# Optimization experiments

Measured on AMD Instinct MI355X. Metric: run time of the kernel, lower is better.

## Reference

```python
import jax, jax.numpy as jnp
import numpy as np

N_NODES = 50000
N_EDGES = 800000
D_IN = 256
D_OUT = 256
N_REL = 8


def setup_inputs() -> dict:
    key = jax.random.key(0)
    k_x, k_ei, k_et, k_w = jax.random.split(key, 4)
    x = jax.random.normal(k_x, (N_NODES, D_IN), dtype=jnp.float32)
    edge_index = jax.random.randint(k_ei, (2, N_EDGES), 0, N_NODES, dtype=jnp.int32)
    edge_type = jax.random.randint(k_et, (N_EDGES,), 0, N_REL, dtype=jnp.int32)
    # xavier_uniform-style init for per-relation weights [R, I, O]
    limit = float(np.sqrt(6.0 / (D_IN + D_OUT)))
    weight = jax.random.uniform(k_w, (N_REL, D_IN, D_OUT), dtype=jnp.float32,
                                minval=-limit, maxval=limit)
    bias = jnp.zeros((D_OUT,), dtype=jnp.float32)
    return {"x": x, "edge_index": edge_index, "edge_type": edge_type,
            "weight": weight, "bias": bias}


def reference(x, edge_index, edge_type, weight, bias):
    # RGCN (block / per-relation weights):
    #   out[row] += x[col] @ weight[edge_type]
    # Vectorized: transform every node under every relation once (dense GEMM),
    # then gather the right (relation, col) slice per edge and scatter-add to row.
    num_nodes = x.shape[0]
    row, col = edge_index[0], edge_index[1]
    xt = jnp.einsum('ni,rio->rno', x, weight)          # [R, N, O]
    messages = xt[edge_type, col]                       # [E, O]
    out = jax.ops.segment_sum(messages, row, num_segments=num_nodes)  # [N, O]
    return jax.nn.relu(out + bias)
```

## Files before the change

kernel.cpp:

```cpp
#include <hip/hip_runtime.h>
#include <hip/hip_bf16.h>
#include <stdint.h>

typedef __attribute__((ext_vector_type(8))) short short8;
typedef __attribute__((ext_vector_type(4))) float f32x4;

#define D 256
#define NTY 4

static __device__ __forceinline__ float b2f(unsigned short u) {
  union { unsigned u; float f; } c; c.u = ((unsigned)u) << 16; return c.f;
}
static __device__ __forceinline__ unsigned short f2b(float f) {
  union { float f; unsigned u; } c; c.f = f;
  unsigned r = (c.u + 0x7FFFu + ((c.u >> 16) & 1u)) >> 16;
  return (unsigned short)r;
}

static __device__ __forceinline__ void gload16(const void* g, void* l) {
  __builtin_amdgcn_global_load_lds(
      (const __attribute__((address_space(1))) unsigned int*)g,
      (__attribute__((address_space(3))) unsigned int*)l, 16, 0, 0);
}

__global__ void k_cvt_xw(const float* __restrict__ x, unsigned short* __restrict__ xb,
                         long n_elems, long pad_elems, int xblocks,
                         const float* __restrict__ w, unsigned short* __restrict__ wt) {
  if (blockIdx.x < (unsigned)xblocks) {
    long i4 = (long)blockIdx.x * 256 + threadIdx.x;
    if (i4 * 4 >= pad_elems) return;
    ushort4 o;
    if (i4 * 4 < n_elems) {
      float4 v = ((const float4*)x)[i4];
      o.x = f2b(v.x); o.y = f2b(v.y); o.z = f2b(v.z); o.w = f2b(v.w);
    } else {
      o.x = 0; o.y = 0; o.z = 0; o.w = 0;
    }
    ((ushort4*)xb)[i4] = o;
  } else {
    int t = (blockIdx.x - xblocks) * 256 + threadIdx.x;
    int i = t & 255;
    int orow = t >> 8;
    int r = orow >> 8, o = orow & 255;
    wt[t] = f2b(w[((size_t)(r * 256 + i)) * 256 + o]);
  }
}

__global__ __launch_bounds__(256) void k_gemm(const unsigned short* __restrict__ A,
                                              const unsigned short* __restrict__ B,
                                              unsigned short* __restrict__ C,
                                              int ldc) {
  __shared__ __align__(16) char lA[64 * 512];
  __shared__ __align__(16) char lB[128 * 128];
  const int t = threadIdx.x;
  const int lane = t & 63;
  const int wave = t >> 6;
  const int l15 = lane & 15, lhi = lane >> 4;
  const size_t tm = (size_t)blockIdx.x * 64;
  const int y0 = blockIdx.y * NTY;

#pragma unroll
  for (int it = 0; it < 8; ++it) {
    int s = it * 256 + t;
    int row = s >> 5, c = s & 31;
    gload16(A + (tm + row) * 256 + ((c ^ (row & 7)) * 8),
            lA + (it * 256 + wave * 64) * 16);
  }

  for (int y = y0; y < y0 + NTY; ++y) {
    const int tn = y * 128;
    f32x4 acc[4][2];
#pragma unroll
    for (int a = 0; a < 4; ++a)
#pragma unroll
      for (int b = 0; b < 2; ++b)
#pragma unroll
        for (int e = 0; e < 4; ++e) acc[a][b][e] = 0.f;

    for (int kt = 0; kt < 256; kt += 64) {
      __syncthreads();
#pragma unroll
      for (int it = 0; it < 4; ++it) {
        int s = it * 256 + t;
        int row = s >> 3, c = s & 7;
        gload16(B + (tn + row) * 256 + kt + ((c ^ (row & 7)) * 8),
                lB + (it * 256 + wave * 64) * 16);
      }
      __syncthreads();

      short8 af[4][2], bfv[2][2];
      const int ktc = kt >> 3;
#pragma unroll
      for (int mi = 0; mi < 4; ++mi) {
#pragma unroll
        for (int kk = 0; kk < 2; ++kk) {
          int R = mi * 16 + l15;
          int c = ktc + kk * 4 + lhi;
          af[mi][kk] = *(const short8*)(lA + R * 512 + ((c ^ (R & 7)) * 16));
        }
      }
#pragma unroll
      for (int ni = 0; ni < 2; ++ni) {
#pragma unroll
        for (int kk = 0; kk < 2; ++kk) {
          int R2 = wave * 32 + ni * 16 + l15;
          int c2 = kk * 4 + lhi;
          bfv[ni][kk] = *(const short8*)(lB + R2 * 128 + ((c2 ^ (R2 & 7)) * 16));
        }
      }
#pragma unroll
      for (int mi = 0; mi < 4; ++mi) {
#pragma unroll
        for (int ni = 0; ni < 2; ++ni) {
          acc[mi][ni] = __builtin_amdgcn_mfma_f32_16x16x32_bf16(af[mi][0], bfv[ni][0], acc[mi][ni], 0, 0, 0);
          acc[mi][ni] = __builtin_amdgcn_mfma_f32_16x16x32_bf16(af[mi][1], bfv[ni][1], acc[mi][ni], 0, 0, 0);
        }
      }
    }
#pragma unroll
    for (int mi = 0; mi < 4; ++mi) {
#pragma unroll
      for (int j = 0; j < 4; ++j) {
        size_t row = tm + mi * 16 + lhi * 4 + j;
        unsigned pk = (unsigned)f2b(acc[mi][0][j]) | ((unsigned)f2b(acc[mi][1][j]) << 16);
        *(unsigned*)(C + row * (size_t)ldc + tn + wave * 32 + l15 * 2) = pk;
      }
    }
  }
}

__global__ void k_deg(const int* __restrict__ ei, int* deg, int E) {
  int e = blockIdx.x * 256 + threadIdx.x;
  if (e < E) atomicAdd(&deg[ei[e]], 1);
}
__global__ void k_scan1(const int* __restrict__ deg, int* bsum, int n) {
  __shared__ int sm[256];
  int t = threadIdx.x, idx = blockIdx.x * 256 + t;
  sm[t] = idx < n ? deg[idx] : 0;
  __syncthreads();
  for (int off = 128; off; off >>= 1) {
    if (t < off) sm[t] += sm[t + off];
    __syncthreads();
  }
  if (t == 0) bsum[blockIdx.x] = sm[0];
}
__global__ void k_scan23(const int* __restrict__ deg, const int* __restrict__ bsum,
                         int* rowptr, int* cursor, int nsc, int n) {
  __shared__ int sb[256];
  __shared__ int sm[256];
  int t = threadIdx.x, idx = blockIdx.x * 256 + t;
  int bv = t < nsc ? bsum[t] : 0;
  sb[t] = bv;
  __syncthreads();
  for (int off = 1; off < 256; off <<= 1) {
    int x = t >= off ? sb[t - off] : 0;
    __syncthreads();
    sb[t] += x;
    __syncthreads();
  }
  int v = idx < n ? deg[idx] : 0;
  sm[t] = v;
  __syncthreads();
  for (int off = 1; off < 256; off <<= 1) {
    int x = t >= off ? sm[t - off] : 0;
    __syncthreads();
    sm[t] += x;
    __syncthreads();
  }
  int boff = sb[blockIdx.x] - bsum[blockIdx.x];
  if (idx < n) {
    int e = boff + sm[t] - v;
    rowptr[idx] = e;
    cursor[idx] = e;
  }
  if (blockIdx.x == 0 && t == 0) rowptr[n] = sb[nsc - 1];
}
__global__ void k_bin(const int* __restrict__ ei, const int* __restrict__ et,
                      int* cursor, unsigned* ect, int E) {
  int e = blockIdx.x * 256 + threadIdx.x;
  if (e >= E) return;
  int r = ei[e], c = ei[E + e], ty = et[e];
  int pos = atomicAdd(&cursor[r], 1);
  ect[pos] = (unsigned)c | ((unsigned)ty << 20);
}

__global__ __launch_bounds__(256) void k_gather(const unsigned* __restrict__ ect,
                                                const int* __restrict__ rowptr,
                                                const unsigned short* __restrict__ xt,
                                                const float* __restrict__ bias,
                                                float* __restrict__ out, int n, int ldxt) {
  __shared__ float sm[4][256];
  const int lane = threadIdx.x & 63;
  const int wid = threadIdx.x >> 6;
  const int h = lane >> 5;
  const int sl = lane & 31;
  const int row = blockIdx.x * 4 + wid;
  if (row >= n) return;
  const int s = rowptr[row], e = rowptr[row + 1];
  const int cnt = e - s;
  float a[8] = {0.f, 0.f, 0.f, 0.f, 0.f, 0.f, 0.f, 0.f};
  unsigned myct = (s + lane < e) ? ect[s + lane] : 0u;
  int c1 = cnt > 64 ? 64 : cnt;
  for (int i = 0; i < c1; i += 2) {
    int j = i + h;
    unsigned ct = __shfl(myct, j);
    if (j < c1) {
      size_t base = (size_t)(ct & 0xFFFFFu) * ldxt + ((ct >> 20) << 8) + (sl << 3);
      short8 v = *(const short8*)(xt + base);
#pragma unroll
      for (int k = 0; k < 8; ++k) a[k] += b2f((unsigned short)v[k]);
    }
  }
  for (int i = s + 64; i < e; i += 2) {
    int j = i + h;
    if (j < e) {
      unsigned ct = ect[j];
      size_t base = (size_t)(ct & 0xFFFFFu) * ldxt + ((ct >> 20) << 8) + (sl << 3);
      short8 v = *(const short8*)(xt + base);
#pragma unroll
      for (int k = 0; k < 8; ++k) a[k] += b2f((unsigned short)v[k]);
    }
  }
#pragma unroll
  for (int k = 0; k < 8; ++k) a[k] += __shfl_xor(a[k], 32);
  if (h == 0) {
#pragma unroll
    for (int k = 0; k < 8; ++k) {
      int p8 = sl * 8 + k;
      int o = (p8 & 224) | ((p8 & 1) << 4) | ((p8 & 31) >> 1);
      sm[wid][o] = a[k];
    }
  }
  float4 v = *(const float4*)&sm[wid][lane * 4];
  float4 bb = ((const float4*)bias)[lane];
  float4 o;
  o.x = fmaxf(v.x + bb.x, 0.f);
  o.y = fmaxf(v.y + bb.y, 0.f);
  o.z = fmaxf(v.z + bb.z, 0.f);
  o.w = fmaxf(v.w + bb.w, 0.f);
  ((float4*)out)[(size_t)row * 64 + lane] = o;
}

extern "C" void kernel_launch(void* const* d_in, const int* in_sizes, int n_in,
                              void* d_out, int out_size, void* d_ws, size_t ws_size,
                              hipStream_t stream) {
  const float* x = (const float*)d_in[0];
  const int* ei = (const int*)d_in[1];
  const int* et = (const int*)d_in[2];
  const float* w = (const float*)d_in[3];
  const float* bias = (const float*)d_in[4];
  float* out = (float*)d_out;

  const int Nn = in_sizes[0] / D;
  const int E = in_sizes[2];
  const int R = in_sizes[3] / (D * D);
  const int Mpad = ((Nn + 63) / 64) * 64;
  const int NC = R * D;

  char* p = (char*)d_ws;
  auto alloc = [&](size_t bytes) -> char* {
    char* q = p;
    p += (bytes + 255) & ~(size_t)255;
    return q;
  };
  unsigned short* xt = (unsigned short*)alloc((size_t)Mpad * NC * 2);
  unsigned short* xb = (unsigned short*)alloc((size_t)Mpad * D * 2);
  unsigned short* wt = (unsigned short*)alloc((size_t)NC * D * 2);
  int* rowptr = (int*)alloc((size_t)(Nn + 1) * 4);
  int* cursor = (int*)alloc((size_t)Nn * 4);
  int* deg = (int*)alloc((size_t)Nn * 4);
  int* bsum = (int*)alloc(1024);
  unsigned* ect = (unsigned*)alloc((size_t)E * 4);

  const int nsc = (Nn + 255) / 256;
  const int xblocks = Mpad / 4;

  hipMemsetAsync(deg, 0, (size_t)Nn * 4, stream);
  hipLaunchKernelGGL(k_deg, dim3((E + 255) / 256), dim3(256), 0, stream, ei, deg, E);
  hipLaunchKernelGGL(k_scan1, dim3(nsc), dim3(256), 0, stream, deg, bsum, Nn);
  hipLaunchKernelGGL(k_scan23, dim3(nsc), dim3(256), 0, stream, deg, bsum,
                     rowptr, cursor, nsc, Nn);
  hipLaunchKernelGGL(k_bin, dim3((E + 255) / 256), dim3(256), 0, stream, ei, et, cursor, ect, E);

  hipLaunchKernelGGL(k_cvt_xw, dim3(xblocks + (NC * D) / 256), dim3(256), 0, stream,
                     x, xb, (long)Nn * D, (long)Mpad * D, xblocks, w, wt);
  hipLaunchKernelGGL(k_gemm, dim3(Mpad / 64, NC / (128 * NTY)), dim3(256), 0, stream,
                     xb, wt, xt, NC);

  hipLaunchKernelGGL(k_gather, dim3((Nn + 3) / 4), dim3(256), 0, stream, ect, rowptr,
                     xt, bias, out, Nn, NC);
}
```

Before: 356.2 us.

## Aggregate per relation before transform and fuse gather with per-relation GEMM

Reorders the computation from transform-then-gather to gather-then-transform. Edges are binned by (destination, relation) in a CSR built over N*R keys. A fused kernel sums bf16 input rows per relation for 32 destination nodes, stages them in LDS, and multiplies by that relation's weight with MFMA, accumulating across all 8 relations. This removes the large [N, R*256] bf16 intermediate write and its random re-read. The costs are an 8x larger degree/scan array, a serial per-thread edge loop inside the GEMM kernel, an extra bf16 rounding of the partial sums, and reloading the full weight matrix for every 32-row block.

```diff
diff --git a/kernel.cpp b/kernel.cpp
--- a/kernel.cpp
+++ b/kernel.cpp
@@ -6,15 +6,13 @@
 typedef __attribute__((ext_vector_type(4))) float f32x4;
 
 #define D 256
-#define NTY 4
 
 static __device__ __forceinline__ float b2f(unsigned short u) {
   union { unsigned u; float f; } c; c.u = ((unsigned)u) << 16; return c.f;
 }
-static __device__ __forceinline__ unsigned short f2b(float f) {
+static __device__ __forceinline__ unsigned f2b(float f) {
   union { float f; unsigned u; } c; c.f = f;
-  unsigned r = (c.u + 0x7FFFu + ((c.u >> 16) & 1u)) >> 16;
-  return (unsigned short)r;
+  return (c.u + 0x7FFFu + ((c.u >> 16) & 1u)) >> 16;
 }
 
 static __device__ __forceinline__ void gload16(const void* g, void* l) {
@@ -42,203 +40,191 @@
     int i = t & 255;
     int orow = t >> 8;
     int r = orow >> 8, o = orow & 255;
-    wt[t] = f2b(w[((size_t)(r * 256 + i)) * 256 + o]);
-  }
-}
-
-__global__ __launch_bounds__(256) void k_gemm(const unsigned short* __restrict__ A,
-                                              const unsigned short* __restrict__ B,
-                                              unsigned short* __restrict__ C,
-                                              int ldc) {
-  __shared__ __align__(16) char lA[64 * 512];
-  __shared__ __align__(16) char lB[128 * 128];
+    wt[t] = (unsigned short)f2b(w[((size_t)(r * 256 + i)) * 256 + o]);
+  }
+}
+
+__global__ void k_deg2(const int* __restrict__ ei, const int* __restrict__ et,
+                       int* deg, int E) {
+  int e = blockIdx.x * 256 + threadIdx.x;
+  if (e < E) atomicAdd(&deg[ei[e] * 8 + et[e]], 1);
+}
+__global__ void k_scan1(const int* __restrict__ deg, int* bsum, int n) {
+  __shared__ int sm[256];
+  int t = threadIdx.x, idx = blockIdx.x * 256 + t;
+  sm[t] = idx < n ? deg[idx] : 0;
+  __syncthreads();
+  for (int off = 128; off; off >>= 1) {
+    if (t < off) sm[t] += sm[t + off];
+    __syncthreads();
+  }
+  if (t == 0) bsum[blockIdx.x] = sm[0];
+}
+__global__ void k_scan2b(const int* __restrict__ bsum, int* __restrict__ boff,
+                         int* __restrict__ rp_end, int nsc) {
+  __shared__ int sm[256];
+  int t = threadIdx.x;
+  int loc[8];
+  int s = 0;
+#pragma unroll
+  for (int j = 0; j < 8; ++j) {
+    int idx = t * 8 + j;
+    loc[j] = s;
+    s += (idx < nsc) ? bsum[idx] : 0;
+  }
+  sm[t] = s;
+  __syncthreads();
+  for (int off = 1; off < 256; off <<= 1) {
+    int x = t >= off ? sm[t - off] : 0;
+    __syncthreads();
+    sm[t] += x;
+    __syncthreads();
+  }
+  int base = sm[t] - s;
+#pragma unroll
+  for (int j = 0; j < 8; ++j) {
+    int idx = t * 8 + j;
+    if (idx < nsc) boff[idx] = base + loc[j];
+  }
+  if (t == 255) *rp_end = sm[255];
+}
+__global__ void k_scan3(const int* __restrict__ deg, const int* __restrict__ boff,
+                        int* rowptr, int* cursor, int n) {
+  __shared__ int sm[256];
+  int t = threadIdx.x, idx = blockIdx.x * 256 + t;
+  int v = idx < n ? deg[idx] : 0;
+  sm[t] = v;
+  __syncthreads();
+  for (int off = 1; off < 256; off <<= 1) {
+    int x = t >= off ? sm[t - off] : 0;
+    __syncthreads();
+    sm[t] += x;
+    __syncthreads();
+  }
+  if (idx < n) {
+    int e = boff[blockIdx.x] + sm[t] - v;
+    rowptr[idx] = e;
+    cursor[idx] = e;
+  }
+}
+__global__ void k_bin2(const int* __restrict__ ei, const int* __restrict__ et,
+                       int* cursor, int* ecol, int E) {
+  int e = blockIdx.x * 256 + threadIdx.x;
+  if (e >= E) return;
+  int key = ei[e] * 8 + et[e];
+  int pos = atomicAdd(&cursor[key], 1);
+  ecol[pos] = ei[E + e];
+}
+
+__global__ __launch_bounds__(256) void k_fused(const unsigned short* __restrict__ xb,
+                                               const unsigned short* __restrict__ Wt,
+                                               const int* __restrict__ rp2,
+                                               const int* __restrict__ ecol,
+                                               const float* __restrict__ bias,
+                                               float* __restrict__ out, int Nn) {
+  __shared__ __align__(16) char lds[32 * 512 + 256 * 128];
+  char* lH = lds;
+  char* lB = lds + 32 * 512;
   const int t = threadIdx.x;
   const int lane = t & 63;
   const int wave = t >> 6;
   const int l15 = lane & 15, lhi = lane >> 4;
-  const size_t tm = (size_t)blockIdx.x * 64;
-  const int y0 = blockIdx.y * NTY;
-
-#pragma unroll
-  for (int it = 0; it < 8; ++it) {
-    int s = it * 256 + t;
-    int row = s >> 5, c = s & 31;
-    gload16(A + (tm + row) * 256 + ((c ^ (row & 7)) * 8),
-            lA + (it * 256 + wave * 64) * 16);
-  }
-
-  for (int y = y0; y < y0 + NTY; ++y) {
-    const int tn = y * 128;
-    f32x4 acc[4][2];
-#pragma unroll
-    for (int a = 0; a < 4; ++a)
-#pragma unroll
-      for (int b = 0; b < 2; ++b)
-#pragma unroll
-        for (int e = 0; e < 4; ++e) acc[a][b][e] = 0.f;
-
+  const int half = lane >> 5, sl = lane & 31;
+  const int tm = blockIdx.x * 32;
+
+  f32x4 acc[2][4];
+#pragma unroll
+  for (int a = 0; a < 2; ++a)
+#pragma unroll
+    for (int b = 0; b < 4; ++b)
+#pragma unroll
+      for (int e = 0; e < 4; ++e) acc[a][b][e] = 0.f;
+
+  for (int r = 0; r < 8; ++r) {
+    __syncthreads();
+#pragma unroll
+    for (int pr = 0; pr < 4; ++pr) {
+      int hr = wave * 8 + pr * 2 + half;
+      int row = tm + hr;
+      float a[8] = {0.f, 0.f, 0.f, 0.f, 0.f, 0.f, 0.f, 0.f};
+      if (row < Nn) {
+        int key = row * 8 + r;
+        int s = rp2[key], e = rp2[key + 1];
+        for (int i = s; i < e; ++i) {
+          int col = ecol[i];
+          short8 v = *(const short8*)(xb + (size_t)col * 256 + sl * 8);
+#pragma unroll
+          for (int k = 0; k < 8; ++k) a[k] += b2f((unsigned short)v[k]);
+        }
+      }
+      uint4 pk;
+      pk.x = f2b(a[0]) | (f2b(a[1]) << 16);
+      pk.y = f2b(a[2]) | (f2b(a[3]) << 16);
+      pk.z = f2b(a[4]) | (f2b(a[5]) << 16);
+      pk.w = f2b(a[6]) | (f2b(a[7]) << 16);
+      *(uint4*)(lH + hr * 512 + ((sl ^ (hr & 7)) * 16)) = pk;
+    }
     for (int kt = 0; kt < 256; kt += 64) {
       __syncthreads();
 #pragma unroll
-      for (int it = 0; it < 4; ++it) {
-        int s = it * 256 + t;
-        int row = s >> 3, c = s & 7;
-        gload16(B + (tn + row) * 256 + kt + ((c ^ (row & 7)) * 8),
+      for (int it = 0; it < 8; ++it) {
+        int s2 = it * 256 + t;
+        int nrow = s2 >> 3, c = s2 & 7;
+        gload16(Wt + ((size_t)(r * 256 + nrow)) * 256 + kt + ((c ^ (nrow & 7)) * 8),
                 lB + (it * 256 + wave * 64) * 16);
       }
       __syncthreads();
 
-      short8 af[4][2], bfv[2][2];
       const int ktc = kt >> 3;
-#pragma unroll
-      for (int mi = 0; mi < 4; ++mi) {
+      short8 af[2][2];
+#pragma unroll
+      for (int mi = 0; mi < 2; ++mi)
 #pragma unroll
         for (int kk = 0; kk < 2; ++kk) {
           int R = mi * 16 + l15;
           int c = ktc + kk * 4 + lhi;
-          af[mi][kk] = *(const short8*)(lA + R * 512 + ((c ^ (R & 7)) * 16));
+          af[mi][kk] = *(const short8*)(lH + R * 512 + ((c ^ (R & 7)) * 16));
+        }
+#pragma unroll
+      for (int ni = 0; ni < 4; ++ni) {
+        int R2 = wave * 64 + ni * 16 + l15;
+        short8 b0 = *(const short8*)(lB + R2 * 128 + ((lhi ^ (R2 & 7)) * 16));
+        short8 b1 = *(const short8*)(lB + R2 * 128 + (((4 + lhi) ^ (R2 & 7)) * 16));
+#pragma unroll
+        for (int mi = 0; mi < 2; ++mi) {
+          acc[mi][ni] = __builtin_amdgcn_mfma_f32_16x16x32_bf16(af[mi][0], b0, acc[mi][ni], 0, 0, 0);
+          acc[mi][ni] = __builtin_amdgcn_mfma_f32_16x16x32_bf16(af[mi][1], b1, acc[mi][ni], 0, 0, 0);
         }
       }
-#pragma unroll
-      for (int ni = 0; ni < 2; ++ni) {
-#pragma unroll
-        for (int kk = 0; kk < 2; ++kk) {
-          int R2 = wave * 32 + ni * 16 + l15;
-          int c2 = kk * 4 + lhi;
-          bfv[ni][kk] = *(const short8*)(lB + R2 * 128 + ((c2 ^ (R2 & 7)) * 16));
-        }
-      }
-#pragma unroll
-      for (int mi = 0; mi < 4; ++mi) {
-#pragma unroll
-        for (int ni = 0; ni < 2; ++ni) {
-          acc[mi][ni] = __builtin_amdgcn_mfma_f32_16x16x32_bf16(af[mi][0], bfv[ni][0], acc[mi][ni], 0, 0, 0);
-          acc[mi][ni] = __builtin_amdgcn_mfma_f32_16x16x32_bf16(af[mi][1], bfv[ni][1], acc[mi][ni], 0, 0, 0);
-        }
-      }
-    }
-#pragma unroll
-    for (int mi = 0; mi < 4; ++mi) {
-#pragma unroll
-      for (int j = 0; j < 4; ++j) {
-        size_t row = tm + mi * 16 + lhi * 4 + j;
-        unsigned pk = (unsigned)f2b(acc[mi][0][j]) | ((unsigned)f2b(acc[mi][1][j]) << 16);
-        *(unsigned*)(C + row * (size_t)ldc + tn + wave * 32 + l15 * 2) = pk;
-      }
-    }
-  }
-}
-
-__global__ void k_deg(const int* __restrict__ ei, int* deg, int E) {
-  int e = blockIdx.x * 256 + threadIdx.x;
-  if (e < E) atomicAdd(&deg[ei[e]], 1);
-}
-__global__ void k_scan1(const int* __restrict__ deg, int* bsum, int n) {
-  __shared__ int sm[256];
-  int t = threadIdx.x, idx = blockIdx.x * 256 + t;
-  sm[t] = idx < n ? deg[idx] : 0;
-  __syncthreads();
-  for (int off = 128; off; off >>= 1) {
-    if (t < off) sm[t] += sm[t + off];
-    __syncthreads();
-  }
-  if (t == 0) bsum[blockIdx.x] = sm[0];
-}
-__global__ void k_scan23(const int* __restrict__ deg, const int* __restrict__ bsum,
-                         int* rowptr, int* cursor, int nsc, int n) {
-  __shared__ int sb[256];
-  __shared__ int sm[256];
-  int t = threadIdx.x, idx = blockIdx.x * 256 + t;
-  int bv = t < nsc ? bsum[t] : 0;
-  sb[t] = bv;
-  __syncthreads();
-  for (int off = 1; off < 256; off <<= 1) {
-    int x = t >= off ? sb[t - off] : 0;
-    __syncthreads();
-    sb[t] += x;
-    __syncthreads();
-  }
-  int v = idx < n ? deg[idx] : 0;
-  sm[t] = v;
-  __syncthreads();
-  for (int off = 1; off < 256; off <<= 1) {
-    int x = t >= off ? sm[t - off] : 0;
-    __syncthreads();
-    sm[t] += x;
-    __syncthreads();
-  }
-  int boff = sb[blockIdx.x] - bsum[blockIdx.x];
-  if (idx < n) {
-    int e = boff + sm[t] - v;
-    rowptr[idx] = e;
-    cursor[idx] = e;
-  }
-  if (blockIdx.x == 0 && t == 0) rowptr[n] = sb[nsc - 1];
-}
-__global__ void k_bin(const int* __restrict__ ei, const int* __restrict__ et,
-                      int* cursor, unsigned* ect, int E) {
-  int e = blockIdx.x * 256 + threadIdx.x;
-  if (e >= E) return;
-  int r = ei[e], c = ei[E + e], ty = et[e];
-  int pos = atomicAdd(&cursor[r], 1);
-  ect[pos] = (unsigned)c | ((unsigned)ty << 20);
-}
-
-__global__ __launch_bounds__(256) void k_gather(const unsigned* __restrict__ ect,
-                                                const int* __restrict__ rowptr,
-                                                const unsigned short* __restrict__ xt,
-                                                const float* __restrict__ bias,
-                                                float* __restrict__ out, int n, int ldxt) {
-  __shared__ float sm[4][256];
-  const int lane = threadIdx.x & 63;
-  const int wid = threadIdx.x >> 6;
-  const int h = lane >> 5;
-  const int sl = lane & 31;
-  const int row = blockIdx.x * 4 + wid;
-  if (row >= n) return;
-  const int s = rowptr[row], e = rowptr[row + 1];
-  const int cnt = e - s;
-  float a[8] = {0.f, 0.f, 0.f, 0.f, 0.f, 0.f, 0.f, 0.f};
-  unsigned myct = (s + lane < e) ? ect[s + lane] : 0u;
-  int c1 = cnt > 64 ? 64 : cnt;
-  for (int i = 0; i < c1; i += 2) {
-    int j = i + h;
-    unsigned ct = __shfl(myct, j);
-    if (j < c1) {
-      size_t base = (size_t)(ct & 0xFFFFFu) * ldxt + ((ct >> 20) << 8) + (sl << 3);
-      short8 v = *(const short8*)(xt + base);
-#pragma unroll
-      for (int k = 0; k < 8; ++k) a[k] += b2f((unsigned short)v[k]);
-    }
-  }
-  for (int i = s + 64; i < e; i += 2) {
-    int j = i + h;
-    if (j < e) {
-      unsigned ct = ect[j];
-      size_t base = (size_t)(ct & 0xFFFFFu) * ldxt + ((ct >> 20) << 8) + (sl << 3);
-      short8 v = *(const short8*)(xt + base);
-#pragma unroll
-      for (int k = 0; k < 8; ++k) a[k] += b2f((unsigned short)v[k]);
-    }
-  }
-#pragma unroll
-  for (int k = 0; k < 8; ++k) a[k] += __shfl_xor(a[k], 32);
-  if (h == 0) {
-#pragma unroll
-    for (int k = 0; k < 8; ++k) {
-      int p8 = sl * 8 + k;
-      int o = (p8 & 224) | ((p8 & 1) << 4) | ((p8 & 31) >> 1);
-      sm[wid][o] = a[k];
-    }
-  }
-  float4 v = *(const float4*)&sm[wid][lane * 4];
-  float4 bb = ((const float4*)bias)[lane];
-  float4 o;
-  o.x = fmaxf(v.x + bb.x, 0.f);
-  o.y = fmaxf(v.y + bb.y, 0.f);
-  o.z = fmaxf(v.z + bb.z, 0.f);
-  o.w = fmaxf(v.w + bb.w, 0.f);
-  ((float4*)out)[(size_t)row * 64 + lane] = o;
+    }
+  }
+  __syncthreads();
+  float* bz = (float*)lds;
+#pragma unroll
+  for (int mi = 0; mi < 2; ++mi)
+#pragma unroll
+    for (int ni = 0; ni < 4; ++ni)
+#pragma unroll
+      for (int j = 0; j < 4; ++j)
+        bz[(mi * 16 + lhi * 4 + j) * 260 + wave * 64 + ni * 16 + l15] = acc[mi][ni][j];
+  __syncthreads();
+  const float4* b4 = (const float4*)bias;
+#pragma unroll
+  for (int it = 0; it < 8; ++it) {
+    int idx = it * 256 + t;
+    int r32 = idx >> 6, seg = idx & 63;
+    int row = tm + r32;
+    if (row < Nn) {
+      float4 v = *(const float4*)(bz + r32 * 260 + seg * 4);
+      float4 bb = b4[seg];
+      float4 o;
+      o.x = fmaxf(v.x + bb.x, 0.f);
+      o.y = fmaxf(v.y + bb.y, 0.f);
+      o.z = fmaxf(v.z + bb.z, 0.f);
+      o.w = fmaxf(v.w + bb.w, 0.f);
+      ((float4*)out)[(size_t)row * 64 + seg] = o;
+    }
+  }
 }
 
 extern "C" void kernel_launch(void* const* d_in, const int* in_sizes, int n_in,
@@ -254,8 +240,10 @@
   const int Nn = in_sizes[0] / D;
   const int E = in_sizes[2];
   const int R = in_sizes[3] / (D * D);
-  const int Mpad = ((Nn + 63) / 64) * 64;
+  const int M32 = (Nn + 31) / 32;
+  const int Mpad = M32 * 32;
   const int NC = R * D;
+  const int n2 = Nn * R;
 
   char* p = (char*)d_ws;
   auto alloc = [&](size_t bytes) -> char* {
@@ -263,30 +251,28 @@
     p += (bytes + 255) & ~(size_t)255;
     return q;
   };
-  unsigned short* xt = (unsigned short*)alloc((size_t)Mpad * NC * 2);
   unsigned short* xb = (unsigned short*)alloc((size_t)Mpad * D * 2);
   unsigned short* wt = (unsigned short*)alloc((size_t)NC * D * 2);
-  int* rowptr = (int*)alloc((size_t)(Nn + 1) * 4);
-  int* cursor = (int*)alloc((size_t)Nn * 4);
-  int* deg = (int*)alloc((size_t)Nn * 4);
-  int* bsum = (int*)alloc(1024);
-  unsigned* ect = (unsigned*)alloc((size_t)E * 4);
-
-  const int nsc = (Nn + 255) / 256;
+  int* rp2 = (int*)alloc((size_t)(n2 + 1) * 4);
+  int* cursor2 = (int*)alloc((size_t)n2 * 4);
+  int* deg2 = (int*)alloc((size_t)n2 * 4);
+  int* bsum = (int*)alloc(2048 * 4);
+  int* boff = (int*)alloc(2048 * 4);
+  int* ecol = (int*)alloc((size_t)E * 4);
+
+  const int nsc2 = (n2 + 255) / 256;
   const int xblocks = Mpad / 4;
 
-  hipMemsetAsync(deg, 0, (size_t)Nn * 4, stream);
-  hipLaunchKernelGGL(k_deg, dim3((E + 255) / 256), dim3(256), 0, stream, ei, deg, E);
-  hipLaunchKernelGGL(k_scan1, dim3(nsc), dim3(256), 0, stream, deg, bsum, Nn);
-  hipLaunchKernelGGL(k_scan23, dim3(nsc), dim3(256), 0, stream, deg, bsum,
-                     rowptr, cursor, nsc, Nn);
-  hipLaunchKernelGGL(k_bin, dim3((E + 255) / 256), dim3(256), 0, stream, ei, et, cursor, ect, E);
+  hipMemsetAsync(deg2, 0, (size_t)n2 * 4, stream);
+  hipLaunchKernelGGL(k_deg2, dim3((E + 255) / 256), dim3(256), 0, stream, ei, et, deg2, E);
+  hipLaunchKernelGGL(k_scan1, dim3(nsc2), dim3(256), 0, stream, deg2, bsum, n2);
+  hipLaunchKernelGGL(k_scan2b, dim3(1), dim3(256), 0, stream, bsum, boff, rp2 + n2, nsc2);
+  hipLaunchKernelGGL(k_scan3, dim3(nsc2), dim3(256), 0, stream, deg2, boff, rp2, cursor2, n2);
+  hipLaunchKernelGGL(k_bin2, dim3((E + 255) / 256), dim3(256), 0, stream, ei, et, cursor2, ecol, E);
 
   hipLaunchKernelGGL(k_cvt_xw, dim3(xblocks + (NC * D) / 256), dim3(256), 0, stream,
                      x, xb, (long)Nn * D, (long)Mpad * D, xblocks, w, wt);
-  hipLaunchKernelGGL(k_gemm, dim3(Mpad / 64, NC / (128 * NTY)), dim3(256), 0, stream,
-                     xb, wt, xt, NC);
-
-  hipLaunchKernelGGL(k_gather, dim3((Nn + 3) / 4), dim3(256), 0, stream, ect, rowptr,
-                     xt, bias, out, Nn, NC);
-}
+
+  hipLaunchKernelGGL(k_fused, dim3(M32), dim3(256), 0, stream, xb, wt, rp2, ecol,
+                     bias, out, Nn);
+}
```

Result: slower. 475.8 us (+33.6%).

## Fuse CSR build and bf16 conversion into one cooperative grid-synced kernel

Applied to the files above, without the earlier changes.

Replaces the memset plus five separate preprocessing kernels (degree count, two scan passes, binning, x/w conversion) with a single cooperative kernel of 1024 blocks that uses grid-wide syncs between phases. The aim is to cut kernel launch and inter-kernel gap overhead. In exchange it adds five grid barriers, and the edge and conversion loops become grid-stride with a fixed grid size, which may lower parallelism compared with the original launch sizes.

```diff
diff --git a/kernel.cpp b/kernel.cpp
--- a/kernel.cpp
+++ b/kernel.cpp
@@ -1,6 +1,9 @@
 #include <hip/hip_runtime.h>
 #include <hip/hip_bf16.h>
+#include <hip/hip_cooperative_groups.h>
 #include <stdint.h>
+
+namespace cg = cooperative_groups;
 
 typedef __attribute__((ext_vector_type(8))) short short8;
 typedef __attribute__((ext_vector_type(4))) float f32x4;
@@ -11,10 +14,9 @@
 static __device__ __forceinline__ float b2f(unsigned short u) {
   union { unsigned u; float f; } c; c.u = ((unsigned)u) << 16; return c.f;
 }
-static __device__ __forceinline__ unsigned short f2b(float f) {
+static __device__ __forceinline__ unsigned f2b(float f) {
   union { float f; unsigned u; } c; c.f = f;
-  unsigned r = (c.u + 0x7FFFu + ((c.u >> 16) & 1u)) >> 16;
-  return (unsigned short)r;
+  return (c.u + 0x7FFFu + ((c.u >> 16) & 1u)) >> 16;
 }
 
 static __device__ __forceinline__ void gload16(const void* g, void* l) {
@@ -23,12 +25,21 @@
       (__attribute__((address_space(3))) unsigned int*)l, 16, 0, 0);
 }
 
-__global__ void k_cvt_xw(const float* __restrict__ x, unsigned short* __restrict__ xb,
-                         long n_elems, long pad_elems, int xblocks,
-                         const float* __restrict__ w, unsigned short* __restrict__ wt) {
-  if (blockIdx.x < (unsigned)xblocks) {
-    long i4 = (long)blockIdx.x * 256 + threadIdx.x;
-    if (i4 * 4 >= pad_elems) return;
+__global__ __launch_bounds__(256) void k_prep(
+    const float* __restrict__ x, unsigned short* __restrict__ xb,
+    long n_elems, long pad_elems,
+    const float* __restrict__ w, unsigned short* __restrict__ wt, int wtot,
+    const int* __restrict__ ei, const int* __restrict__ et, int E,
+    int* deg, int* bsum, int* boff, int* rowptr, int* cursor,
+    unsigned* ect, int Nn, int nsc) {
+  cg::grid_group grid = cg::this_grid();
+  __shared__ int sm[256];
+  const int t = threadIdx.x;
+  const int gtid = blockIdx.x * 256 + t;
+  const int gsz = gridDim.x * 256;
+
+  for (int i = gtid; i < Nn; i += gsz) deg[i] = 0;
+  for (long i4 = gtid; i4 * 4 < pad_elems; i4 += gsz) {
     ushort4 o;
     if (i4 * 4 < n_elems) {
       float4 v = ((const float4*)x)[i4];
@@ -37,12 +48,68 @@
       o.x = 0; o.y = 0; o.z = 0; o.w = 0;
     }
     ((ushort4*)xb)[i4] = o;
-  } else {
-    int t = (blockIdx.x - xblocks) * 256 + threadIdx.x;
-    int i = t & 255;
-    int orow = t >> 8;
+  }
+  for (int q = gtid; q < wtot; q += gsz) {
+    int i = q & 255;
+    int orow = q >> 8;
     int r = orow >> 8, o = orow & 255;
-    wt[t] = f2b(w[((size_t)(r * 256 + i)) * 256 + o]);
+    wt[q] = (unsigned short)f2b(w[((size_t)(r * 256 + i)) * 256 + o]);
+  }
+  grid.sync();
+
+  for (int e = gtid; e < E; e += gsz) atomicAdd(&deg[ei[e]], 1);
+  grid.sync();
+
+  if (blockIdx.x < (unsigned)nsc) {
+    int idx = blockIdx.x * 256 + t;
+    sm[t] = idx < Nn ? deg[idx] : 0;
+    __syncthreads();
+    for (int off = 128; off; off >>= 1) {
+      if (t < off) sm[t] += sm[t + off];
+      __syncthreads();
+    }
+    if (t == 0) bsum[blockIdx.x] = sm[0];
+  }
+  grid.sync();
+
+  if (blockIdx.x == 0) {
+    int v = t < nsc ? bsum[t] : 0;
+    sm[t] = v;
+    __syncthreads();
+    for (int off = 1; off < 256; off <<= 1) {
+      int xv = t >= off ? sm[t - off] : 0;
+      __syncthreads();
+      sm[t] += xv;
+      __syncthreads();
+    }
+    if (t < nsc) boff[t] = sm[t] - v;
+    if (t == nsc - 1) rowptr[Nn] = sm[t];
+  }
+  grid.sync();
+
+  if (blockIdx.x < (unsigned)nsc) {
+    int idx = blockIdx.x * 256 + t;
+    int v = idx < Nn ? deg[idx] : 0;
+    sm[t] = v;
+    __syncthreads();
+    for (int off = 1; off < 256; off <<= 1) {
+      int xv = t >= off ? sm[t - off] : 0;
+      __syncthreads();
+      sm[t] += xv;
+      __syncthreads();
+    }
+    if (idx < Nn) {
+      int e0 = boff[blockIdx.x] + sm[t] - v;
+      rowptr[idx] = e0;
+      cursor[idx] = e0;
+    }
+  }
+  grid.sync();
+
+  for (int e = gtid; e < E; e += gsz) {
+    int r = ei[e], c = ei[E + e], ty = et[e];
+    int pos = atomicAdd(&cursor[r], 1);
+    ect[pos] = (unsigned)c | ((unsigned)ty << 20);
   }
 }
 
@@ -122,66 +189,11 @@
 #pragma unroll
       for (int j = 0; j < 4; ++j) {
         size_t row = tm + mi * 16 + lhi * 4 + j;
-        unsigned pk = (unsigned)f2b(acc[mi][0][j]) | ((unsigned)f2b(acc[mi][1][j]) << 16);
+        unsigned pk = f2b(acc[mi][0][j]) | (f2b(acc[mi][1][j]) << 16);
         *(unsigned*)(C + row * (size_t)ldc + tn + wave * 32 + l15 * 2) = pk;
       }
     }
   }
-}
-
-__global__ void k_deg(const int* __restrict__ ei, int* deg, int E) {
-  int e = blockIdx.x * 256 + threadIdx.x;
-  if (e < E) atomicAdd(&deg[ei[e]], 1);
-}
-__global__ void k_scan1(const int* __restrict__ deg, int* bsum, int n) {
-  __shared__ int sm[256];
-  int t = threadIdx.x, idx = blockIdx.x * 256 + t;
-  sm[t] = idx < n ? deg[idx] : 0;
-  __syncthreads();
-  for (int off = 128; off; off >>= 1) {
-    if (t < off) sm[t] += sm[t + off];
-    __syncthreads();
-  }
-  if (t == 0) bsum[blockIdx.x] = sm[0];
-}
-__global__ void k_scan23(const int* __restrict__ deg, const int* __restrict__ bsum,
-                         int* rowptr, int* cursor, int nsc, int n) {
-  __shared__ int sb[256];
-  __shared__ int sm[256];
-  int t = threadIdx.x, idx = blockIdx.x * 256 + t;
-  int bv = t < nsc ? bsum[t] : 0;
-  sb[t] = bv;
-  __syncthreads();
-  for (int off = 1; off < 256; off <<= 1) {
-    int x = t >= off ? sb[t - off] : 0;
-    __syncthreads();
-    sb[t] += x;
-    __syncthreads();
-  }
-  int v = idx < n ? deg[idx] : 0;
-  sm[t] = v;
-  __syncthreads();
-  for (int off = 1; off < 256; off <<= 1) {
-    int x = t >= off ? sm[t - off] : 0;
-    __syncthreads();
-    sm[t] += x;
-    __syncthreads();
-  }
-  int boff = sb[blockIdx.x] - bsum[blockIdx.x];
-  if (idx < n) {
-    int e = boff + sm[t] - v;
-    rowptr[idx] = e;
-    cursor[idx] = e;
-  }
-  if (blockIdx.x == 0 && t == 0) rowptr[n] = sb[nsc - 1];
-}
-__global__ void k_bin(const int* __restrict__ ei, const int* __restrict__ et,
-                      int* cursor, unsigned* ect, int E) {
-  int e = blockIdx.x * 256 + threadIdx.x;
-  if (e >= E) return;
-  int r = ei[e], c = ei[E + e], ty = et[e];
-  int pos = atomicAdd(&cursor[r], 1);
-  ect[pos] = (unsigned)c | ((unsigned)ty << 20);
 }
 
 __global__ __launch_bounds__(256) void k_gather(const unsigned* __restrict__ ect,
@@ -270,20 +282,22 @@
   int* cursor = (int*)alloc((size_t)Nn * 4);
   int* deg = (int*)alloc((size_t)Nn * 4);
   int* bsum = (int*)alloc(1024);
+  int* boff = (int*)alloc(1024);
   unsigned* ect = (unsigned*)alloc((size_t)E * 4);
 
   const int nsc = (Nn + 255) / 256;
-  const int xblocks = Mpad / 4;
-
-  hipMemsetAsync(deg, 0, (size_t)Nn * 4, stream);
-  hipLaunchKernelGGL(k_deg, dim3((E + 255) / 256), dim3(256), 0, stream, ei, deg, E);
-  hipLaunchKernelGGL(k_scan1, dim3(nsc), dim3(256), 0, stream, deg, bsum, Nn);
-  hipLaunchKernelGGL(k_scan23, dim3(nsc), dim3(256), 0, stream, deg, bsum,
-                     rowptr, cursor, nsc, Nn);
-  hipLaunchKernelGGL(k_bin, dim3((E + 255) / 256), dim3(256), 0, stream, ei, et, cursor, ect, E);
-
-  hipLaunchKernelGGL(k_cvt_xw, dim3(xblocks + (NC * D) / 256), dim3(256), 0, stream,
-                     x, xb, (long)Nn * D, (long)Mpad * D, xblocks, w, wt);
+  long n_elems = (long)Nn * D;
+  long pad_elems = (long)Mpad * D;
+  int wtot = NC * D;
+  int E_ = E, Nn_ = Nn, nsc_ = nsc;
+
+  void* args[] = {(void*)&x, (void*)&xb, (void*)&n_elems, (void*)&pad_elems,
+                  (void*)&w, (void*)&wt, (void*)&wtot,
+                  (void*)&ei, (void*)&et, (void*)&E_,
+                  (void*)&deg, (void*)&bsum, (void*)&boff, (void*)&rowptr,
+                  (void*)&cursor, (void*)&ect, (void*)&Nn_, (void*)&nsc_};
+  hipLaunchCooperativeKernel((void*)k_prep, dim3(1024), dim3(256), args, 0, stream);
+
   hipLaunchKernelGGL(k_gemm, dim3(Mpad / 64, NC / (128 * NTY)), dim3(256), 0, stream,
                      xb, wt, xt, NC);
 
```

After: 915.8 us. 2.57x slower.

## Merge degree count into conversion kernel and edge binning into GEMM launch

Applied to the files above, without the earlier changes.

Folds the degree-counting atomics into the bf16 conversion kernel and the edge-binning pass into the GEMM kernel as extra blocks of each grid, cutting the launch count from 7 to 5. Independent work now shares a launch, so the atomic-heavy scatter blocks can overlap with the conversion and GEMM blocks instead of running serially. The GEMM block index is now decoded from a 1D grid assuming NC/(128*NTY) == 4. Binning blocks in the GEMM launch allocate the GEMM's shared memory even though they do not use it, which may limit how many of them are resident at once.

```diff
diff --git a/kernel.cpp b/kernel.cpp
--- a/kernel.cpp
+++ b/kernel.cpp
@@ -11,10 +11,9 @@
 static __device__ __forceinline__ float b2f(unsigned short u) {
   union { unsigned u; float f; } c; c.u = ((unsigned)u) << 16; return c.f;
 }
-static __device__ __forceinline__ unsigned short f2b(float f) {
+static __device__ __forceinline__ unsigned f2b(float f) {
   union { float f; unsigned u; } c; c.f = f;
-  unsigned r = (c.u + 0x7FFFu + ((c.u >> 16) & 1u)) >> 16;
-  return (unsigned short)r;
+  return (c.u + 0x7FFFu + ((c.u >> 16) & 1u)) >> 16;
 }
 
 static __device__ __forceinline__ void gload16(const void* g, void* l) {
@@ -23,11 +22,14 @@
       (__attribute__((address_space(3))) unsigned int*)l, 16, 0, 0);
 }
 
-__global__ void k_cvt_xw(const float* __restrict__ x, unsigned short* __restrict__ xb,
-                         long n_elems, long pad_elems, int xblocks,
-                         const float* __restrict__ w, unsigned short* __restrict__ wt) {
-  if (blockIdx.x < (unsigned)xblocks) {
-    long i4 = (long)blockIdx.x * 256 + threadIdx.x;
+__global__ void k_cvt_deg(const float* __restrict__ x, unsigned short* __restrict__ xb,
+                          long n_elems, long pad_elems, int xblocks,
+                          const float* __restrict__ w, unsigned short* __restrict__ wt,
+                          int wblocks,
+                          const int* __restrict__ ei, int* deg, int E) {
+  int bx = blockIdx.x;
+  if (bx < xblocks) {
+    long i4 = (long)bx * 256 + threadIdx.x;
     if (i4 * 4 >= pad_elems) return;
     ushort4 o;
     if (i4 * 4 < n_elems) {
@@ -37,102 +39,18 @@
       o.x = 0; o.y = 0; o.z = 0; o.w = 0;
     }
     ((ushort4*)xb)[i4] = o;
-  } else {
-    int t = (blockIdx.x - xblocks) * 256 + threadIdx.x;
+  } else if (bx < xblocks + wblocks) {
+    int t = (bx - xblocks) * 256 + threadIdx.x;
     int i = t & 255;
     int orow = t >> 8;
     int r = orow >> 8, o = orow & 255;
-    wt[t] = f2b(w[((size_t)(r * 256 + i)) * 256 + o]);
-  }
-}
-
-__global__ __launch_bounds__(256) void k_gemm(const unsigned short* __restrict__ A,
-                                              const unsigned short* __restrict__ B,
-                                              unsigned short* __restrict__ C,
-                                              int ldc) {
-  __shared__ __align__(16) char lA[64 * 512];
-  __shared__ __align__(16) char lB[128 * 128];
-  const int t = threadIdx.x;
-  const int lane = t & 63;
-  const int wave = t >> 6;
-  const int l15 = lane & 15, lhi = lane >> 4;
-  const size_t tm = (size_t)blockIdx.x * 64;
-  const int y0 = blockIdx.y * NTY;
-
-#pragma unroll
-  for (int it = 0; it < 8; ++it) {
-    int s = it * 256 + t;
-    int row = s >> 5, c = s & 31;
-    gload16(A + (tm + row) * 256 + ((c ^ (row & 7)) * 8),
-            lA + (it * 256 + wave * 64) * 16);
-  }
-
-  for (int y = y0; y < y0 + NTY; ++y) {
-    const int tn = y * 128;
-    f32x4 acc[4][2];
-#pragma unroll
-    for (int a = 0; a < 4; ++a)
-#pragma unroll
-      for (int b = 0; b < 2; ++b)
-#pragma unroll
-        for (int e = 0; e < 4; ++e) acc[a][b][e] = 0.f;
-
-    for (int kt = 0; kt < 256; kt += 64) {
-      __syncthreads();
-#pragma unroll
-      for (int it = 0; it < 4; ++it) {
-        int s = it * 256 + t;
-        int row = s >> 3, c = s & 7;
-        gload16(B + (tn + row) * 256 + kt + ((c ^ (row & 7)) * 8),
-                lB + (it * 256 + wave * 64) * 16);
-      }
-      __syncthreads();
-
-      short8 af[4][2], bfv[2][2];
-      const int ktc = kt >> 3;
-#pragma unroll
-      for (int mi = 0; mi < 4; ++mi) {
-#pragma unroll
-        for (int kk = 0; kk < 2; ++kk) {
-          int R = mi * 16 + l15;
-          int c = ktc + kk * 4 + lhi;
-          af[mi][kk] = *(const short8*)(lA + R * 512 + ((c ^ (R & 7)) * 16));
-        }
-      }
-#pragma unroll
-      for (int ni = 0; ni < 2; ++ni) {
-#pragma unroll
-        for (int kk = 0; kk < 2; ++kk) {
-          int R2 = wave * 32 + ni * 16 + l15;
-          int c2 = kk * 4 + lhi;
-          bfv[ni][kk] = *(const short8*)(lB + R2 * 128 + ((c2 ^ (R2 & 7)) * 16));
-        }
-      }
-#pragma unroll
-      for (int mi = 0; mi < 4; ++mi) {
-#pragma unroll
-        for (int ni = 0; ni < 2; ++ni) {
-          acc[mi][ni] = __builtin_amdgcn_mfma_f32_16x16x32_bf16(af[mi][0], bfv[ni][0], acc[mi][ni], 0, 0, 0);
-          acc[mi][ni] = __builtin_amdgcn_mfma_f32_16x16x32_bf16(af[mi][1], bfv[ni][1], acc[mi][ni], 0, 0, 0);
-        }
-      }
-    }
-#pragma unroll
-    for (int mi = 0; mi < 4; ++mi) {
-#pragma unroll
-      for (int j = 0; j < 4; ++j) {
-        size_t row = tm + mi * 16 + lhi * 4 + j;
-        unsigned pk = (unsigned)f2b(acc[mi][0][j]) | ((unsigned)f2b(acc[mi][1][j]) << 16);
-        *(unsigned*)(C + row * (size_t)ldc + tn + wave * 32 + l15 * 2) = pk;
-      }
-    }
-  }
-}
-
-__global__ void k_deg(const int* __restrict__ ei, int* deg, int E) {
-  int e = blockIdx.x * 256 + threadIdx.x;
-  if (e < E) atomicAdd(&deg[ei[e]], 1);
-}
+    wt[t] = (unsigned short)f2b(w[((size_t)(r * 256 + i)) * 256 + o]);
+  } else {
+    int e = (bx - xblocks - wblocks) * 256 + threadIdx.x;
+    if (e < E) atomicAdd(&deg[ei[e]], 1);
+  }
+}
+
 __global__ void k_scan1(const int* __restrict__ deg, int* bsum, int n) {
   __shared__ int sm[256];
   int t = threadIdx.x, idx = blockIdx.x * 256 + t;
@@ -175,13 +93,99 @@
   }
   if (blockIdx.x == 0 && t == 0) rowptr[n] = sb[nsc - 1];
 }
-__global__ void k_bin(const int* __restrict__ ei, const int* __restrict__ et,
-                      int* cursor, unsigned* ect, int E) {
-  int e = blockIdx.x * 256 + threadIdx.x;
-  if (e >= E) return;
-  int r = ei[e], c = ei[E + e], ty = et[e];
-  int pos = atomicAdd(&cursor[r], 1);
-  ect[pos] = (unsigned)c | ((unsigned)ty << 20);
+
+__global__ __launch_bounds__(256) void k_gemm_bin(
+    const unsigned short* __restrict__ A, const unsigned short* __restrict__ B,
+    unsigned short* __restrict__ C, int ldc, int gemmBlocks,
+    const int* __restrict__ ei, const int* __restrict__ et,
+    int* cursor, unsigned* ect, int E) {
+  __shared__ __align__(16) char lA[64 * 512];
+  __shared__ __align__(16) char lB[128 * 128];
+  const int bx = blockIdx.x;
+  if (bx >= gemmBlocks) {
+    int e = (bx - gemmBlocks) * 256 + threadIdx.x;
+    if (e < E) {
+      int r = ei[e], c = ei[E + e], ty = et[e];
+      int pos = atomicAdd(&cursor[r], 1);
+      ect[pos] = (unsigned)c | ((unsigned)ty << 20);
+    }
+    return;
+  }
+  const int t = threadIdx.x;
+  const int lane = t & 63;
+  const int wave = t >> 6;
+  const int l15 = lane & 15, lhi = lane >> 4;
+  const size_t tm = (size_t)(bx >> 2) * 64;
+  const int y0 = (bx & 3) * NTY;
+
+#pragma unroll
+  for (int it = 0; it < 8; ++it) {
+    int s = it * 256 + t;
+    int row = s >> 5, c = s & 31;
+    gload16(A + (tm + row) * 256 + ((c ^ (row & 7)) * 8),
+            lA + (it * 256 + wave * 64) * 16);
+  }
+
+  for (int y = y0; y < y0 + NTY; ++y) {
+    const int tn = y * 128;
+    f32x4 acc[4][2];
+#pragma unroll
+    for (int a = 0; a < 4; ++a)
+#pragma unroll
+      for (int b = 0; b < 2; ++b)
+#pragma unroll
+        for (int e = 0; e < 4; ++e) acc[a][b][e] = 0.f;
+
+    for (int kt = 0; kt < 256; kt += 64) {
+      __syncthreads();
+#pragma unroll
+      for (int it = 0; it < 4; ++it) {
+        int s = it * 256 + t;
+        int row = s >> 3, c = s & 7;
+        gload16(B + (tn + row) * 256 + kt + ((c ^ (row & 7)) * 8),
+                lB + (it * 256 + wave * 64) * 16);
+      }
+      __syncthreads();
+
+      short8 af[4][2], bfv[2][2];
+      const int ktc = kt >> 3;
+#pragma unroll
+      for (int mi = 0; mi < 4; ++mi) {
+#pragma unroll
+        for (int kk = 0; kk < 2; ++kk) {
+          int R = mi * 16 + l15;
+          int c = ktc + kk * 4 + lhi;
+          af[mi][kk] = *(const short8*)(lA + R * 512 + ((c ^ (R & 7)) * 16));
+        }
+      }
+#pragma unroll
+      for (int ni = 0; ni < 2; ++ni) {
+#pragma unroll
+        for (int kk = 0; kk < 2; ++kk) {
+          int R2 = wave * 32 + ni * 16 + l15;
+          int c2 = kk * 4 + lhi;
+          bfv[ni][kk] = *(const short8*)(lB + R2 * 128 + ((c2 ^ (R2 & 7)) * 16));
+        }
+      }
+#pragma unroll
+      for (int mi = 0; mi < 4; ++mi) {
+#pragma unroll
+        for (int ni = 0; ni < 2; ++ni) {
+          acc[mi][ni] = __builtin_amdgcn_mfma_f32_16x16x32_bf16(af[mi][0], bfv[ni][0], acc[mi][ni], 0, 0, 0);
+          acc[mi][ni] = __builtin_amdgcn_mfma_f32_16x16x32_bf16(af[mi][1], bfv[ni][1], acc[mi][ni], 0, 0, 0);
+        }
+      }
+    }
+#pragma unroll
+    for (int mi = 0; mi < 4; ++mi) {
+#pragma unroll
+      for (int j = 0; j < 4; ++j) {
+        size_t row = tm + mi * 16 + lhi * 4 + j;
+        unsigned pk = f2b(acc[mi][0][j]) | (f2b(acc[mi][1][j]) << 16);
+        *(unsigned*)(C + row * (size_t)ldc + tn + wave * 32 + l15 * 2) = pk;
+      }
+    }
+  }
 }
 
 __global__ __launch_bounds__(256) void k_gather(const unsigned* __restrict__ ect,
@@ -274,19 +278,20 @@
 
   const int nsc = (Nn + 255) / 256;
   const int xblocks = Mpad / 4;
+  const int wblocks = (NC * D) / 256;
+  const int eblocks = (E + 255) / 256;
+  const int gemmBlocks = (Mpad / 64) * 4;
 
   hipMemsetAsync(deg, 0, (size_t)Nn * 4, stream);
-  hipLaunchKernelGGL(k_deg, dim3((E + 255) / 256), dim3(256), 0, stream, ei, deg, E);
+
+  hipLaunchKernelGGL(k_cvt_deg, dim3(xblocks + wblocks + eblocks), dim3(256), 0, stream,
+                     x, xb, (long)Nn * D, (long)Mpad * D, xblocks,
+                     w, wt, wblocks, ei, deg, E);
   hipLaunchKernelGGL(k_scan1, dim3(nsc), dim3(256), 0, stream, deg, bsum, Nn);
   hipLaunchKernelGGL(k_scan23, dim3(nsc), dim3(256), 0, stream, deg, bsum,
                      rowptr, cursor, nsc, Nn);
-  hipLaunchKernelGGL(k_bin, dim3((E + 255) / 256), dim3(256), 0, stream, ei, et, cursor, ect, E);
-
-  hipLaunchKernelGGL(k_cvt_xw, dim3(xblocks + (NC * D) / 256), dim3(256), 0, stream,
-                     x, xb, (long)Nn * D, (long)Mpad * D, xblocks, w, wt);
-  hipLaunchKernelGGL(k_gemm, dim3(Mpad / 64, NC / (128 * NTY)), dim3(256), 0, stream,
-                     xb, wt, xt, NC);
-
+  hipLaunchKernelGGL(k_gemm_bin, dim3(gemmBlocks + eblocks), dim3(256), 0, stream,
+                     xb, wt, xt, NC, gemmBlocks, ei, et, cursor, ect, E);
   hipLaunchKernelGGL(k_gather, dim3((Nn + 3) / 4), dim3(256), 0, stream, ect, rowptr,
                      xt, bias, out, Nn, NC);
 }
```

New measurement: 347.6 us. 1.02x faster.
